# Optimization experiments

Measured on AMD Instinct MI355X. Metric: run time of the kernel, lower is better.

The kernel has to match this reference:

```python
import jax, jax.numpy as jnp
import numpy as np
from jax import lax

EPS = 1e-8
ROUTINGS = 3


def squash(u, axis=-1):
    norm = jnp.linalg.norm(u, axis=axis, keepdims=True)
    scale = norm ** 2 / (1 + norm ** 2) / (norm + EPS)
    return scale * u


def conv2d(x, w, b, stride):
    y = lax.conv_general_dilated(x, w, window_strides=(stride, stride), padding='VALID',
                                 dimension_numbers=('NCHW', 'OIHW', 'NCHW'))
    return y + b[None, :, None, None]


def setup_inputs() -> dict:
    key = jax.random.key(0)
    ks = jax.random.split(key, 6)
    x = jax.random.normal(ks[0], (512, 1, 28, 28), dtype=jnp.float32)
    conv1_w = 0.1 * jax.random.normal(ks[1], (256, 1, 9, 9), dtype=jnp.float32)
    conv1_b = 0.1 * jax.random.normal(ks[2], (256,), dtype=jnp.float32)
    pc_w = 0.01 * jax.random.normal(ks[3], (256, 256, 9, 9), dtype=jnp.float32)
    pc_b = 0.01 * jax.random.normal(ks[4], (256,), dtype=jnp.float32)
    caps_w = 0.01 * jax.random.normal(ks[5], (10, 1152, 16, 8), dtype=jnp.float32)
    return {"x": x, "conv1_w": conv1_w, "conv1_b": conv1_b,
            "pc_w": pc_w, "pc_b": pc_b, "caps_w": caps_w}


def reference(x, conv1_w, conv1_b, pc_w, pc_b, caps_w):
    B = x.shape[0]
    # conv1 + relu: [B,1,28,28] -> [B,256,20,20]
    h = jax.nn.relu(conv2d(x, conv1_w, conv1_b, stride=1))
    # primary capsules: [B,256,20,20] -> [B,256,6,6] -> [B,1152,8], squash
    h = conv2d(h, pc_w, pc_b, stride=2)
    u = squash(h.reshape(B, 1152, 8))
    # votes: weight [O,I,Do,Di] x u [B,I,Di] -> x_hat [B,O,I,Do]
    x_hat = jnp.einsum('oidk,bik->boid', caps_w, u)
    x_hat_det = lax.stop_gradient(x_hat)
    b_logits = jnp.zeros((B, caps_w.shape[0], caps_w.shape[1]), dtype=x_hat.dtype)
    out_caps = None
    for i in range(ROUTINGS):
        c = jax.nn.softmax(b_logits, axis=1)  # softmax over output caps
        if i == ROUTINGS - 1:
            out_caps = squash(jnp.sum(c[..., None] * x_hat, axis=2))  # [B,O,Do]
        else:
            v = squash(jnp.sum(c[..., None] * x_hat_det, axis=2))  # [B,O,Do]
            b_logits = b_logits + jnp.einsum('bod,boid->boi', v, x_hat_det)
    length = jnp.linalg.norm(out_caps, axis=-1)  # [B,O]
    return length
```

## Files before the change

kernel.cpp:

```cpp
#include <hip/hip_runtime.h>
#include <hip/hip_bf16.h>
#include <hip/hip_fp16.h>
#include <math.h>

#define EPS 1e-8f

typedef __attribute__((ext_vector_type(8))) short bf16x8;
typedef __attribute__((ext_vector_type(8))) _Float16 f16x8;
typedef __attribute__((ext_vector_type(4))) float f32x4;

__device__ static inline unsigned short f2bf(float f) {
    __hip_bfloat16 h = __float2bfloat16(f);
    return *reinterpret_cast<unsigned short*>(&h);
}
__device__ static inline unsigned short f2h(float f) {
    __half h = __float2half(f);
    return *reinterpret_cast<unsigned short*>(&h);
}

__device__ static inline void gld_lds16(const void* g, void* l) {
    __builtin_amdgcn_global_load_lds((const __attribute__((address_space(1))) void*)g,
                                     (__attribute__((address_space(3))) void*)l, 16, 0, 0);
}

__device__ static inline void h8tof(uint4 w, float* f) {
    float2 a = __half22float2(*(__half2*)&w.x);
    float2 b = __half22float2(*(__half2*)&w.y);
    float2 c = __half22float2(*(__half2*)&w.z);
    float2 d = __half22float2(*(__half2*)&w.w);
    f[0] = a.x; f[1] = a.y; f[2] = b.x; f[3] = b.y;
    f[4] = c.x; f[5] = c.y; f[6] = d.x; f[7] = d.y;
}

__global__ void k_cast_x(const float* __restrict__ x, unsigned short* __restrict__ xh) {
    int idx = blockIdx.x * 256 + threadIdx.x;
    if (idx < 401408) xh[idx] = f2h(x[idx]);
}

__global__ void k_tw1h(const float* __restrict__ w1, unsigned short* __restrict__ wt1h) {
    int idx = blockIdx.x * 256 + threadIdx.x;
    if (idx >= 24576) return;
    int n = idx / 96, k = idx % 96;
    wt1h[idx] = (k < 81) ? f2h(w1[n * 81 + k]) : (unsigned short)0;
}

__global__ void k_tw2(const float* __restrict__ pw, unsigned short* __restrict__ wt2t) {
    int idx = blockIdx.x * 256 + threadIdx.x;
    int oc = idx / 20736, k = idx % 20736;
    int q = k >> 8, ic = k & 255;
    wt2t[idx] = f2bf(pw[oc * 20736 + ic * 81 + q]);
}

__global__ void k_cwh(const float* __restrict__ cw, __half* __restrict__ cwh) {
    int idx = blockIdx.x * 256 + threadIdx.x;
    if (idx < 1474560) cwh[idx] = __float2half(cw[idx]);
}

__global__ __launch_bounds__(256) void k_conv1(const unsigned short* __restrict__ xh,
                                               const unsigned short* __restrict__ wt1h,
                                               const float* __restrict__ b1,
                                               unsigned short* __restrict__ h1) {
    __shared__ unsigned short Asm[128 * 104];
    __shared__ unsigned short Bsm[128 * 104];
    const int tid = threadIdx.x;
    const int wave = tid >> 6, lane = tid & 63;
    const int ln15 = lane & 15, quad = lane >> 4;
    const int m0 = blockIdx.x * 128;
    const int n0 = blockIdx.y * 128;
    const int wm = (wave >> 1) * 64, wn = (wave & 1) * 64;

    for (int c = tid; c < 1536; c += 256) {
        int r = c / 12, ch = c % 12;
        uint4 v = *(const uint4*)(wt1h + (size_t)(n0 + r) * 96 + ch * 8);
        *(uint4*)(&Bsm[r * 104 + ch * 8]) = v;
    }
    for (int s = 0; s < 5; ++s) {
        int id = s * 256 + tid;
        if (id < 1152) {
            int m_l = id & 127, kh = id >> 7;
            int m = m0 + m_l;
            int b = m / 400, sp = m % 400;
            int oh = sp / 20, ow = sp % 20;
            const unsigned short* src = xh + b * 784 + (oh + kh) * 28 + ow;
            unsigned short* drow = &Asm[m_l * 104 + kh * 9];
#pragma unroll
            for (int w = 0; w < 9; ++w) drow[w] = src[w];
        }
    }
    for (int z = tid; z < 1920; z += 256) {
        int r = z / 15, kk = 81 + z % 15;
        Asm[r * 104 + kk] = 0;
    }
    __syncthreads();

    f32x4 acc[4][4];
#pragma unroll
    for (int i = 0; i < 4; ++i)
#pragma unroll
        for (int j = 0; j < 4; ++j) acc[i][j] = (f32x4)(0.f);

#pragma unroll
    for (int ks = 0; ks < 3; ++ks) {
        int k0 = (ks * 4 + quad) * 8;
        f16x8 af[4], bfr[4];
#pragma unroll
        for (int i = 0; i < 4; ++i)
            af[i] = *(const f16x8*)&Asm[(wm + i * 16 + ln15) * 104 + k0];
#pragma unroll
        for (int j = 0; j < 4; ++j)
            bfr[j] = *(const f16x8*)&Bsm[(wn + j * 16 + ln15) * 104 + k0];
#pragma unroll
        for (int i = 0; i < 4; ++i)
#pragma unroll
            for (int j = 0; j < 4; ++j)
                acc[i][j] = __builtin_amdgcn_mfma_f32_16x16x32_f16(
                    af[i], bfr[j], acc[i][j], 0, 0, 0);
    }

    float bias[4];
#pragma unroll
    for (int j = 0; j < 4; ++j) bias[j] = b1[n0 + wn + j * 16 + ln15];
#pragma unroll
    for (int i = 0; i < 4; ++i) {
#pragma unroll
        for (int r = 0; r < 4; ++r) {
            int m = m0 + wm + i * 16 + quad * 4 + r;
            unsigned short* dst = h1 + (size_t)m * 256 + n0 + wn;
#pragma unroll
            for (int j = 0; j < 4; ++j) {
                float v = acc[i][j][r] + bias[j];
                dst[j * 16 + ln15] = f2bf(v > 0.f ? v : 0.f);
            }
        }
    }
}

__global__ __launch_bounds__(256) void k_conv2(const unsigned short* __restrict__ h1,
                                               const unsigned short* __restrict__ wt2t,
                                               float* __restrict__ h2a) {
    __shared__ short Asm[128 * 64];
    __shared__ short Bsm[128 * 64];

    const int tid  = threadIdx.x;
    const int wave = tid >> 6, lane = tid & 63;
    const int ln15 = lane & 15, quad = lane >> 4, ln7 = lane & 7;
    const int m0 = blockIdx.x * 128;
    const int n0 = blockIdx.y * 128;
    const int kt0 = blockIdx.z * 81;
    const int wm = (wave >> 1) * 64, wn = (wave & 1) * 64;

    const int rbase = wave * 32 + (lane >> 3);
    const int cswz8 = ((lane & 7) ^ ((lane >> 3) & 7)) * 8;

    size_t aptr[4];
    size_t bptr[4];
#pragma unroll
    for (int s = 0; s < 4; ++s) {
        int r = rbase + s * 8;
        int m = m0 + r;
        int b = m / 36, sp = m % 36;
        int oh = sp / 6, ow = sp % 6;
        aptr[s] = (size_t)((b * 20 + 2 * oh) * 20 + 2 * ow) * 256 + cswz8;
        bptr[s] = (size_t)(n0 + r) * 20736 + cswz8;
    }
    short* alds = &Asm[(wave * 32) * 64 + lane * 8];
    short* blds = &Bsm[(wave * 32) * 64 + lane * 8];

    f32x4 acc[4][4];
#pragma unroll
    for (int i = 0; i < 4; ++i)
#pragma unroll
        for (int j = 0; j < 4; ++j) acc[i][j] = (f32x4)(0.f);

    for (int kt = kt0; kt < kt0 + 81; ++kt) {
        int q = kt >> 2;
        int kh = q / 9, kw = q - kh * 9;
        size_t aoff = (size_t)(kh * 20 + kw) * 256 + ((kt & 3) << 6);
        size_t boff = (size_t)kt << 6;
#pragma unroll
        for (int s = 0; s < 4; ++s)
            gld_lds16(h1 + aptr[s] + aoff, alds + s * 512);
#pragma unroll
        for (int s = 0; s < 4; ++s)
            gld_lds16(wt2t + bptr[s] + boff, blds + s * 512);
        __syncthreads();
#pragma unroll
        for (int ks = 0; ks < 2; ++ks) {
            bf16x8 af[4], bfr[4];
#pragma unroll
            for (int i = 0; i < 4; ++i) {
                int chunk = ((ks << 2) + quad) ^ ln7;
                af[i] = *(const bf16x8*)&Asm[(wm + i * 16 + ln15) * 64 + chunk * 8];
            }
#pragma unroll
            for (int j = 0; j < 4; ++j) {
                int chunk = ((ks << 2) + quad) ^ ln7;
                bfr[j] = *(const bf16x8*)&Bsm[(wn + j * 16 + ln15) * 64 + chunk * 8];
            }
#pragma unroll
            for (int i = 0; i < 4; ++i)
#pragma unroll
                for (int j = 0; j < 4; ++j)
                    acc[i][j] = __builtin_amdgcn_mfma_f32_16x16x32_bf16(
                        af[i], bfr[j], acc[i][j], 0, 0, 0);
        }
        __syncthreads();
    }

    float* zs = h2a + (size_t)blockIdx.z * 4718592;
#pragma unroll
    for (int i = 0; i < 4; ++i) {
#pragma unroll
        for (int r = 0; r < 4; ++r) {
            int m = m0 + wm + i * 16 + quad * 4 + r;
            float* dst = zs + (size_t)m * 256 + n0 + wn;
#pragma unroll
            for (int j = 0; j < 4; ++j)
                dst[j * 16 + ln15] = acc[i][j][r];
        }
    }
}

__global__ __launch_bounds__(256) void k_squash(const float* __restrict__ h2a,
                                                const float* __restrict__ pb,
                                                float* __restrict__ u) {
    __shared__ float tile[36 * 260];
    const int tid = threadIdx.x;
    const int b = blockIdx.x;
    const float* base = h2a + (size_t)b * 36 * 256;
    for (int idx = tid; idx < 9216; idx += 256) {
        int sp = idx >> 8, c = idx & 255;
        float v = pb[c];
#pragma unroll
        for (int z = 0; z < 4; ++z) v += base[(size_t)z * 4718592 + sp * 256 + c];
        tile[sp * 260 + c] = v;
    }
    __syncthreads();
    for (int i2 = tid; i2 < 1152; i2 += 256) {
        int f0 = i2 * 8;
        float val[8];
        float n2 = 0.f;
#pragma unroll
        for (int e = 0; e < 8; ++e) {
            int f = f0 + e;
            int c = f / 36, sp = f - c * 36;
            val[e] = tile[sp * 260 + c];
            n2 += val[e] * val[e];
        }
        float n = sqrtf(n2);
        float s = n2 / (1.f + n2) / (n + EPS);
#pragma unroll
        for (int e = 0; e < 8; ++e) val[e] *= s;
        float* dst = u + (size_t)b * 9216 + f0;
        *(float4*)dst       = *(float4*)val;
        *(float4*)(dst + 4) = *(float4*)(val + 4);
    }
}

__global__ __launch_bounds__(256) void k_xhat(const float* __restrict__ u,
                                              const __half* __restrict__ cwh,
                                              __half* __restrict__ xhat,
                                              float* __restrict__ s0) {
    __shared__ float ush[9216];
    __shared__ float part[4][16];
    const int b = blockIdx.x;
    const int t = threadIdx.x;
    const int wave = t >> 6;
    {
        const float4* src = (const float4*)(u + (size_t)b * 9216);
        float4* dst = (float4*)ush;
        for (int idx = t; idx < 2304; idx += 256) dst[idx] = src[idx];
    }
    __syncthreads();

    for (int o = 0; o < 10; ++o) {
        float s_loc[16];
#pragma unroll
        for (int d = 0; d < 16; ++d) s_loc[d] = 0.f;
        for (int i = t; i < 1152; i += 256) {
            float ui[8];
            *(float4*)ui       = *(const float4*)&ush[i * 8];
            *(float4*)(ui + 4) = *(const float4*)&ush[i * 8 + 4];
            const uint4* wp = (const uint4*)(cwh + ((size_t)(o * 1152 + i) << 7));
            unsigned short xv[16];
#pragma unroll
            for (int d = 0; d < 16; ++d) {
                float f[8];
                h8tof(wp[d], f);
                float xh = f[0] * ui[0] + f[1] * ui[1] + f[2] * ui[2] + f[3] * ui[3]
                         + f[4] * ui[4] + f[5] * ui[5] + f[6] * ui[6] + f[7] * ui[7];
                s_loc[d] += xh;
                xv[d] = f2h(xh);
            }
            __half* dst = xhat + ((size_t)((b * 10 + o) * 1152 + i)) * 16;
            *(uint4*)dst       = *(uint4*)xv;
            *(uint4*)(dst + 8) = *(uint4*)(xv + 8);
        }
#pragma unroll
        for (int off = 32; off > 0; off >>= 1)
#pragma unroll
            for (int d = 0; d < 16; ++d) s_loc[d] += __shfl_down(s_loc[d], off, 64);
        if ((t & 63) == 0) {
#pragma unroll
            for (int d = 0; d < 16; ++d) part[wave][d] = s_loc[d];
        }
        __syncthreads();
        if (t < 16)
            s0[(b * 10 + o) * 16 + t] = part[0][t] + part[1][t] + part[2][t] + part[3][t];
        __syncthreads();
    }
}

__global__ __launch_bounds__(640) void k_routing(const __half* __restrict__ xhat,
                                                 const float* __restrict__ s0,
                                                 float* __restrict__ out) {
    __shared__ float dots[10][1152];
    __shared__ float sv[10][16];
    __shared__ float vsum[10][16];
    __shared__ float scale_sh[10];
    const int t = threadIdx.x;
    const int b = blockIdx.x;
    const int o = t >> 6, lane = t & 63;
    const __half* xb = xhat + ((size_t)(b * 10 + o) * 1152) * 16;

    if (t < 160) {
        int oo = t >> 4, d = t & 15;
        sv[oo][d] = 0.1f * s0[(b * 10 + oo) * 16 + d];
    }
    __syncthreads();
    if (t < 10) {
        float n2 = 0.f;
#pragma unroll
        for (int d = 0; d < 16; ++d) n2 += sv[t][d] * sv[t][d];
        float n = sqrtf(n2);
        scale_sh[t] = n2 / (1.f + n2) / (n + EPS);
    }
    __syncthreads();
    if (t < 160) vsum[t >> 4][t & 15] = sv[t >> 4][t & 15] * scale_sh[t >> 4];
    __syncthreads();

    for (int pass = 1; pass <= 2; ++pass) {
        float vs[16];
#pragma unroll
        for (int d = 0; d < 16; ++d) vs[d] = vsum[o][d];
        float s_loc[16];
#pragma unroll
        for (int d = 0; d < 16; ++d) s_loc[d] = 0.f;

        for (int g = 0; g < 6; ++g) {
            uint4 xq[3][2];
#pragma unroll
            for (int j = 0; j < 3; ++j) {
                int i = g * 192 + j * 64 + lane;
                const uint4* p = (const uint4*)(xb + (size_t)i * 16);
                xq[j][0] = p[0];
                xq[j][1] = p[1];
                float f0[8], f1[8];
                h8tof(xq[j][0], f0);
                h8tof(xq[j][1], f1);
                float dd = 0.f;
#pragma unroll
                for (int d = 0; d < 8; ++d) dd += vs[d] * f0[d] + vs[d + 8] * f1[d];
                dots[o][i] = dd;
            }
            __syncthreads();
            if (t < 192) {
                int i = g * 192 + t;
                float dv[10];
#pragma unroll
                for (int oo = 0; oo < 10; ++oo) dv[oo] = dots[oo][i];
                float mx = dv[0];
#pragma unroll
                for (int oo = 1; oo < 10; ++oo) mx = fmaxf(mx, dv[oo]);
                float se = 0.f;
#pragma unroll
                for (int oo = 0; oo < 10; ++oo) { dv[oo] = __expf(dv[oo] - mx); se += dv[oo]; }
                float si = 1.f / se;
#pragma unroll
                for (int oo = 0; oo < 10; ++oo) dots[oo][i] = dv[oo] * si;
            }
            __syncthreads();
#pragma unroll
            for (int j = 0; j < 3; ++j) {
                int i = g * 192 + j * 64 + lane;
                float c = dots[o][i];
                float f0[8], f1[8];
                h8tof(xq[j][0], f0);
                h8tof(xq[j][1], f1);
#pragma unroll
                for (int d = 0; d < 8; ++d) {
                    s_loc[d]     += c * f0[d];
                    s_loc[d + 8] += c * f1[d];
                }
            }
        }
#pragma unroll
        for (int off = 32; off > 0; off >>= 1)
#pragma unroll
            for (int d = 0; d < 16; ++d) s_loc[d] += __shfl_down(s_loc[d], off, 64);
        if (lane == 0) {
#pragma unroll
            for (int d = 0; d < 16; ++d) sv[o][d] = s_loc[d];
        }
        __syncthreads();
        if (pass == 1) {
            if (t < 10) {
                float n2 = 0.f;
#pragma unroll
                for (int d = 0; d < 16; ++d) n2 += sv[t][d] * sv[t][d];
                float n = sqrtf(n2);
                scale_sh[t] = n2 / (1.f + n2) / (n + EPS);
            }
            __syncthreads();
            if (t < 160) {
                int oo = t >> 4, d = t & 15;
                vsum[oo][d] += sv[oo][d] * scale_sh[oo];
            }
            __syncthreads();
        } else {
            if (t < 10) {
                float n2 = 0.f;
#pragma unroll
                for (int d = 0; d < 16; ++d) n2 += sv[t][d] * sv[t][d];
                float n = sqrtf(n2);
                out[b * 10 + t] = (n2 / (1.f + n2)) * (n / (n + EPS));
            }
        }
    }
}

extern "C" void kernel_launch(void* const* d_in, const int* in_sizes, int n_in,
                              void* d_out, int out_size, void* d_ws, size_t ws_size,
                              hipStream_t stream) {
    const float* x  = (const float*)d_in[0];
    const float* w1 = (const float*)d_in[1];
    const float* b1 = (const float*)d_in[2];
    const float* pw = (const float*)d_in[3];
    const float* pb = (const float*)d_in[4];
    const float* cw = (const float*)d_in[5];
    float* out = (float*)d_out;

    char* ws = (char*)d_ws;
    unsigned short* h1   = (unsigned short*)ws;
    float*          h2a  = (float*)(ws + 104857600);
    unsigned short* wt2t = (unsigned short*)(ws + 180355072);
    __half*         xhat = (__half*)ws;
    float*          u    = (float*)(ws + 190971904);
    __half*         cwh  = (__half*)(ws + 209846272);
    unsigned short* xh16 = (unsigned short*)(ws + 212795392);
    unsigned short* wt1h = (unsigned short*)(ws + 213598208);
    float*          s0   = (float*)(ws + 213647360);

    k_cast_x<<<1568, 256, 0, stream>>>(x, xh16);
    k_tw1h<<<96, 256, 0, stream>>>(w1, wt1h);
    k_tw2<<<20736, 256, 0, stream>>>(pw, wt2t);
    k_cwh<<<5760, 256, 0, stream>>>(cw, cwh);
    k_conv1<<<dim3(1600, 2), 256, 0, stream>>>(xh16, wt1h, b1, h1);
    k_conv2<<<dim3(144, 2, 4), 256, 0, stream>>>(h1, wt2t, h2a);
    k_squash<<<512, 256, 0, stream>>>(h2a, pb, u);
    k_xhat<<<512, 256, 0, stream>>>(u, cwh, xhat, s0);
    k_routing<<<512, 640, 0, stream>>>(xhat, s0, out);
}
```

Baseline: 716.1 us.

## Merge prep kernels, reorder conv2 grid, store squashed capsules as fp16

Folds three small conversion kernels (input cast, conv1 weight pad, capsule weight cast) into one launch to cut launch overhead. Remaps the conv2 grid so the N-tile and split-K index vary fastest within each M tile, which may improve L2 reuse of the activation rows. It also replaces the per-iteration divide in the conv2 K loop with incremental kh/kw tracking. The squashed capsule vectors u are now written as fp16 and widened in k_xhat, halving that traffic at some precision cost.

```diff
diff --git a/kernel.cpp b/kernel.cpp
--- a/kernel.cpp
+++ b/kernel.cpp
@@ -32,16 +32,20 @@
     f[4] = c.x; f[5] = c.y; f[6] = d.x; f[7] = d.y;
 }
 
-__global__ void k_cast_x(const float* __restrict__ x, unsigned short* __restrict__ xh) {
+__global__ void k_prep(const float* __restrict__ x, unsigned short* __restrict__ xh,
+                       const float* __restrict__ w1, unsigned short* __restrict__ wt1h,
+                       const float* __restrict__ cw, __half* __restrict__ cwh) {
     int idx = blockIdx.x * 256 + threadIdx.x;
-    if (idx < 401408) xh[idx] = f2h(x[idx]);
-}
-
-__global__ void k_tw1h(const float* __restrict__ w1, unsigned short* __restrict__ wt1h) {
-    int idx = blockIdx.x * 256 + threadIdx.x;
-    if (idx >= 24576) return;
-    int n = idx / 96, k = idx % 96;
-    wt1h[idx] = (k < 81) ? f2h(w1[n * 81 + k]) : (unsigned short)0;
+    if (idx < 401408) {
+        xh[idx] = f2h(x[idx]);
+    } else if (idx < 401408 + 24576) {
+        int j = idx - 401408;
+        int n = j / 96, k = j % 96;
+        wt1h[j] = (k < 81) ? f2h(w1[n * 81 + k]) : (unsigned short)0;
+    } else {
+        int j = idx - 401408 - 24576;
+        cwh[j] = __float2half(cw[j]);
+    }
 }
 
 __global__ void k_tw2(const float* __restrict__ pw, unsigned short* __restrict__ wt2t) {
@@ -49,11 +53,6 @@
     int oc = idx / 20736, k = idx % 20736;
     int q = k >> 8, ic = k & 255;
     wt2t[idx] = f2bf(pw[oc * 20736 + ic * 81 + q]);
-}
-
-__global__ void k_cwh(const float* __restrict__ cw, __half* __restrict__ cwh) {
-    int idx = blockIdx.x * 256 + threadIdx.x;
-    if (idx < 1474560) cwh[idx] = __float2half(cw[idx]);
 }
 
 __global__ __launch_bounds__(256) void k_conv1(const unsigned short* __restrict__ xh,
@@ -144,9 +143,11 @@
     const int tid  = threadIdx.x;
     const int wave = tid >> 6, lane = tid & 63;
     const int ln15 = lane & 15, quad = lane >> 4, ln7 = lane & 7;
-    const int m0 = blockIdx.x * 128;
-    const int n0 = blockIdx.y * 128;
-    const int kt0 = blockIdx.z * 81;
+    const int nz = blockIdx.x;
+    const int n0 = (nz >> 2) * 128;
+    const int zz = nz & 3;
+    const int m0 = blockIdx.y * 128;
+    const int kt0 = zz * 81;
     const int wm = (wave >> 1) * 64, wn = (wave & 1) * 64;
 
     const int rbase = wave * 32 + (lane >> 3);
@@ -172,10 +173,12 @@
 #pragma unroll
         for (int j = 0; j < 4; ++j) acc[i][j] = (f32x4)(0.f);
 
+    int q0 = kt0 >> 2;
+    int kh = q0 / 9, kw = q0 - kh * 9;
+    int pix = (kh * 20 + kw) * 256;
+
     for (int kt = kt0; kt < kt0 + 81; ++kt) {
-        int q = kt >> 2;
-        int kh = q / 9, kw = q - kh * 9;
-        size_t aoff = (size_t)(kh * 20 + kw) * 256 + ((kt & 3) << 6);
+        size_t aoff = (size_t)pix + ((kt & 3) << 6);
         size_t boff = (size_t)kt << 6;
 #pragma unroll
         for (int s = 0; s < 4; ++s)
@@ -205,9 +208,13 @@
                         af[i], bfr[j], acc[i][j], 0, 0, 0);
         }
         __syncthreads();
-    }
-
-    float* zs = h2a + (size_t)blockIdx.z * 4718592;
+        if ((kt & 3) == 3) {
+            if (kw == 8) { kw = 0; ++kh; pix += 12 * 256; }
+            else         { ++kw;       pix += 256; }
+        }
+    }
+
+    float* zs = h2a + (size_t)zz * 4718592;
 #pragma unroll
     for (int i = 0; i < 4; ++i) {
 #pragma unroll
@@ -223,7 +230,7 @@
 
 __global__ __launch_bounds__(256) void k_squash(const float* __restrict__ h2a,
                                                 const float* __restrict__ pb,
-                                                float* __restrict__ u) {
+                                                unsigned short* __restrict__ u) {
     __shared__ float tile[36 * 260];
     const int tid = threadIdx.x;
     const int b = blockIdx.x;
@@ -249,15 +256,14 @@
         }
         float n = sqrtf(n2);
         float s = n2 / (1.f + n2) / (n + EPS);
-#pragma unroll
-        for (int e = 0; e < 8; ++e) val[e] *= s;
-        float* dst = u + (size_t)b * 9216 + f0;
-        *(float4*)dst       = *(float4*)val;
-        *(float4*)(dst + 4) = *(float4*)(val + 4);
-    }
-}
-
-__global__ __launch_bounds__(256) void k_xhat(const float* __restrict__ u,
+        unsigned short o8[8];
+#pragma unroll
+        for (int e = 0; e < 8; ++e) o8[e] = f2h(val[e] * s);
+        *(uint4*)(u + (size_t)b * 9216 + f0) = *(uint4*)o8;
+    }
+}
+
+__global__ __launch_bounds__(256) void k_xhat(const unsigned short* __restrict__ u,
                                               const __half* __restrict__ cwh,
                                               __half* __restrict__ xhat,
                                               float* __restrict__ s0) {
@@ -267,9 +273,11 @@
     const int t = threadIdx.x;
     const int wave = t >> 6;
     {
-        const float4* src = (const float4*)(u + (size_t)b * 9216);
-        float4* dst = (float4*)ush;
-        for (int idx = t; idx < 2304; idx += 256) dst[idx] = src[idx];
+        const uint4* src = (const uint4*)(u + (size_t)b * 9216);
+        for (int idx = t; idx < 1152; idx += 256) {
+            uint4 v = src[idx];
+            h8tof(v, &ush[idx * 8]);
+        }
     }
     __syncthreads();
 
@@ -445,18 +453,16 @@
     float*          h2a  = (float*)(ws + 104857600);
     unsigned short* wt2t = (unsigned short*)(ws + 180355072);
     __half*         xhat = (__half*)ws;
-    float*          u    = (float*)(ws + 190971904);
-    __half*         cwh  = (__half*)(ws + 209846272);
-    unsigned short* xh16 = (unsigned short*)(ws + 212795392);
-    unsigned short* wt1h = (unsigned short*)(ws + 213598208);
-    float*          s0   = (float*)(ws + 213647360);
-
-    k_cast_x<<<1568, 256, 0, stream>>>(x, xh16);
-    k_tw1h<<<96, 256, 0, stream>>>(w1, wt1h);
+    unsigned short* u    = (unsigned short*)(ws + 190971904);
+    __half*         cwh  = (__half*)(ws + 200409088);
+    unsigned short* xh16 = (unsigned short*)(ws + 203358208);
+    unsigned short* wt1h = (unsigned short*)(ws + 204161024);
+    float*          s0   = (float*)(ws + 204210176);
+
+    k_prep<<<7424, 256, 0, stream>>>(x, xh16, w1, wt1h, cw, cwh);
     k_tw2<<<20736, 256, 0, stream>>>(pw, wt2t);
-    k_cwh<<<5760, 256, 0, stream>>>(cw, cwh);
     k_conv1<<<dim3(1600, 2), 256, 0, stream>>>(xh16, wt1h, b1, h1);
-    k_conv2<<<dim3(144, 2, 4), 256, 0, stream>>>(h1, wt2t, h2a);
+    k_conv2<<<dim3(8, 144), 256, 0, stream>>>(h1, wt2t, h2a);
     k_squash<<<512, 256, 0, stream>>>(h2a, pb, u);
     k_xhat<<<512, 256, 0, stream>>>(u, cwh, xhat, s0);
     k_routing<<<512, 640, 0, stream>>>(xhat, s0, out);
```

Measured after the change: 740.0 us. 1.03x slower.
